# Optimization experiments

Measured on AMD Instinct MI355X. Metric: run time of the kernel, lower is better.

The kernel has to match this reference:

```python
import jax, jax.numpy as jnp
import numpy as np

N1, N2 = 8192, 4096
NUM_ITERS = 8  # bounded version of the data-dependent while-loop in Revision_PRED
EPS = 1e-6


def _make_boxes(key, n):
    k1, k2 = jax.random.split(key)
    lt = jax.random.uniform(k1, (n, 2), minval=0.0, maxval=800.0)
    wh = jax.random.uniform(k2, (n, 2), minval=1.0, maxval=200.0)
    return jnp.concatenate([lt, lt + wh], axis=1)  # valid xyxy boxes


def setup_inputs() -> dict:
    key = jax.random.key(0)
    ks = jax.random.split(key, 6)
    return {
        "bboxes1": _make_boxes(ks[0], N1),
        "scores1": jax.random.uniform(ks[1], (N1,)),
        "classes1": jax.random.randint(ks[2], (N1,), 0, 80),
        "bboxes2": _make_boxes(ks[3], N2),
        "scores2": jax.random.uniform(ks[4], (N2,)),
        "classes2": jax.random.randint(ks[5], (N2,), 0, 80),
    }


def bbox_overlaps_iou(b1, b2, eps=EPS):
    # b1: [N1,4], b2: [N2,4] xyxy -> [N1,N2] IoU (mode='iou', is_aligned=False)
    area1 = (b1[:, 2] - b1[:, 0]) * (b1[:, 3] - b1[:, 1])
    area2 = (b2[:, 2] - b2[:, 0]) * (b2[:, 3] - b2[:, 1])
    lt = jnp.maximum(b1[:, None, :2], b2[None, :, :2])
    rb = jnp.minimum(b1[:, None, 2:], b2[None, :, 2:])
    wh = jnp.clip(rb - lt, 0.0)
    overlap = wh[..., 0] * wh[..., 1]
    union = jnp.maximum(area1[:, None] + area2[None, :] - overlap, eps)
    return overlap / union


def reference(bboxes1, scores1, classes1, bboxes2, scores2, classes2):
    # Faithful JAX version of Revision_PRED: pairwise IoU + iterative
    # suppression (index_put_ of 0.5) + scatter of winning predictions.
    ious = bbox_overlaps_iou(bboxes1, bboxes2)
    cols = jnp.arange(ious.shape[1])

    def body(ious, _):
        refine_gt = (ious > 0.5).any(axis=0)            # [N2]
        refine_inds = jnp.argmax(ious, axis=0)          # [N2] best pred per box2
        need_refine = scores1[refine_inds] >= scores2
        lower = refine_gt & (~need_refine)              # == (~refine_gt|~need_refine)&refine_gt
        # index_put_ of 0.5 at (refine_inds[lower], lower cols); no-op elsewhere
        new_vals = jnp.where(lower, 0.5, ious[refine_inds, cols])
        ious = ious.at[refine_inds, cols].set(new_vals)
        return ious, None

    # Bounded, idempotent-once-converged replacement for the `while True` loop.
    ious, _ = jax.lax.scan(body, ious, None, length=NUM_ITERS)

    refine_gt = (ious > 0.5).any(axis=0)
    refine_inds = jnp.argmax(ious, axis=0)
    b2 = jnp.where(refine_gt[:, None], bboxes1[refine_inds], bboxes2)
    s2 = jnp.where(refine_gt, scores1[refine_inds], scores2)
    c2 = jnp.where(refine_gt, classes1[refine_inds], classes2)
    refined_boxes = (b2 + jnp.abs(b2)) * 0.5            # clamp negatives to 0
    missing_mask = (ious < 0.5).all(axis=1)             # preds kept as 'missing'
    return refined_boxes, s2, c2, missing_mask, ious
```

## Files before the change

### kernel.cpp

```cpp
#include <hip/hip_runtime.h>


typedef float vfloat4 __attribute__((ext_vector_type(4)));

constexpr int TOPK = 9;

__device__ __forceinline__ void key_insert(unsigned long long (&t)[TOPK],
                                           unsigned long long pk) {
    if (pk > t[TOPK - 1]) {
#pragma unroll
        for (int j = TOPK - 1; j >= 0; --j) {
            const bool gt_cur  = pk > t[j];
            const bool gt_prev = (j > 0) ? (pk > t[j - 1]) : false;
            if (gt_cur) t[j] = gt_prev ? t[j - 1] : pk;
        }
    }
}

__global__ __launch_bounds__(256) void iou_cand_kernel(
    const float* __restrict__ b1, const float* __restrict__ b2,
    float* __restrict__ ious,
    unsigned int* __restrict__ cnt, unsigned long long* __restrict__ cand,
    unsigned char* __restrict__ rowflag,
    int n1, int n2, int rps, int cap)
{
    const int tid = blockIdx.x * blockDim.x + threadIdx.x;
    const int c0 = tid * 4;
    if (c0 >= n2) return;
    const int r0 = blockIdx.y * rps;
    const int r1 = min(r0 + rps, n1);

    float4 bx[4]; float ar[4];
#pragma unroll
    for (int k = 0; k < 4; ++k) {
        bx[k] = reinterpret_cast<const float4*>(b2)[c0 + k];
        ar[k] = __fmul_rn(__fsub_rn(bx[k].z, bx[k].x),
                          __fsub_rn(bx[k].w, bx[k].y));
    }

    float* orow = ious + (size_t)r0 * n2 + c0;
    for (int r = r0; r < r1; ++r, orow += n2) {
        const float4 p = reinterpret_cast<const float4*>(b1)[r];
        const float a1 = __fmul_rn(__fsub_rn(p.z, p.x), __fsub_rn(p.w, p.y));
        float v[4], ovs[4], uns[4];
#pragma unroll
        for (int k = 0; k < 4; ++k) {
            const float wx = fmaxf(__fsub_rn(fminf(p.z, bx[k].z),
                                             fmaxf(p.x, bx[k].x)), 0.0f);
            const float wy = fmaxf(__fsub_rn(fminf(p.w, bx[k].w),
                                             fmaxf(p.y, bx[k].y)), 0.0f);
            const float ov = __fmul_rn(wx, wy);
            const float un = fmaxf(__fsub_rn(__fadd_rn(a1, ar[k]), ov), 1e-6f);
            ovs[k] = ov; uns[k] = un;
            float rc = __builtin_amdgcn_rcpf(un);
            rc = rc * fmaf(-un, rc, 2.0f);
            v[k] = ov * rc;
        }

        const float vmax = fmaxf(fmaxf(v[0], v[1]), fmaxf(v[2], v[3]));
        if (vmax > 0.499999f) {
#pragma unroll
            for (int k = 0; k < 4; ++k) {
                if (v[k] > 0.499999f) {
                    const float ve = __fdiv_rn(ovs[k], uns[k]);
                    v[k] = ve;
                    if (ve >= 0.5f) {
                        rowflag[r] = 1;
                        if (ve > 0.5f) {
                            const unsigned int idx = atomicAdd(&cnt[c0 + k], 1u);
                            if (idx < (unsigned int)cap)
                                cand[(size_t)idx * n2 + (c0 + k)] =
                                    ((unsigned long long)__float_as_uint(ve) << 32)
                                  | (unsigned long long)(~(unsigned int)r);
                        }
                    }
                }
            }
        }
        vfloat4 vo; vo.x = v[0]; vo.y = v[1]; vo.z = v[2]; vo.w = v[3];
        __builtin_nontemporal_store(vo, reinterpret_cast<vfloat4*>(orow));
    }
}

__global__ __launch_bounds__(64) void refine_missing_kernel(
    const float* __restrict__ b1, const float* __restrict__ s1,
    const int* __restrict__ c1,
    const float* __restrict__ b2, const float* __restrict__ s2,
    const int* __restrict__ c2,
    const unsigned int* __restrict__ cnt,
    const unsigned long long* __restrict__ cand,
    const unsigned char* __restrict__ rowflag,
    float* __restrict__ out_boxes, float* __restrict__ out_s,
    float* __restrict__ out_c, float* __restrict__ out_m,
    float* __restrict__ ious,
    int n1, int n2, int cap)
{
    const int tid = blockIdx.x * blockDim.x + threadIdx.x;

    if (tid < n1)
        out_m[tid] = rowflag[tid] ? 0.0f : 1.0f;

    const int c = tid;
    if (c >= n2) return;

    unsigned long long t[TOPK];
#pragma unroll
    for (int j = 0; j < TOPK; ++j) t[j] = 0ull;

    const int n = (int)cnt[c];
    if (n <= cap) {
        const unsigned long long* L = cand + c;
        for (int e = 0; e < n; ++e)
            key_insert(t, L[(size_t)e * n2]);
    } else {
        for (int r = 0; r < n1; ++r) {
            const float v = ious[(size_t)r * n2 + c];
            if (v > 0.5f)
                key_insert(t, ((unsigned long long)__float_as_uint(v) << 32)
                            | (unsigned long long)(~(unsigned int)r));
        }
    }

    int m = 0;
#pragma unroll
    for (int j = 0; j < TOPK; ++j) m += (t[j] != 0ull) ? 1 : 0;

    int   ti[TOPK];
    float s1v[TOPK];
    const float s2c = s2[c];
#pragma unroll
    for (int j = 0; j < TOPK; ++j) {
        ti[j]  = (int)~(unsigned int)(t[j] & 0xffffffffull);
        s1v[j] = (j < m) ? s1[ti[j]] : 0.0f;
    }

    int k = 0;
#pragma unroll
    for (int j = 0; j < 8; ++j)
        if (j < m && k == j && s1v[j] < s2c) k = j + 1;

#pragma unroll
    for (int j = 0; j < 8; ++j)
        if (j < k) ious[(size_t)ti[j] * n2 + c] = 0.5f;

    const bool refine = (k < m);
    int winner = 0; float wsc = 0.0f;
#pragma unroll
    for (int j = 0; j < TOPK; ++j)
        if (j == k) { winner = ti[j]; wsc = s1v[j]; }

    float4 ob; float os, oc;
    if (refine) {
        ob = reinterpret_cast<const float4*>(b1)[winner];
        os = wsc;
        oc = (float)c1[winner];
    } else {
        ob = reinterpret_cast<const float4*>(b2)[c];
        os = s2c;
        oc = (float)c2[c];
    }
    ob.x = fmaxf(ob.x, 0.0f); ob.y = fmaxf(ob.y, 0.0f);
    ob.z = fmaxf(ob.z, 0.0f); ob.w = fmaxf(ob.w, 0.0f);
    reinterpret_cast<float4*>(out_boxes)[c] = ob;
    out_s[c] = os;
    out_c[c] = oc;
}

extern "C" void kernel_launch(void* const* d_in, const int* in_sizes, int n_in,
                              void* d_out, int out_size, void* d_ws, size_t ws_size,
                              hipStream_t stream) {
    (void)n_in; (void)out_size;
    const float* b1 = (const float*)d_in[0];
    const float* s1 = (const float*)d_in[1];
    const int*   c1 = (const int*)d_in[2];
    const float* b2 = (const float*)d_in[3];
    const float* s2 = (const float*)d_in[4];
    const int*   c2 = (const int*)d_in[5];
    const int n1 = in_sizes[1];
    const int n2 = in_sizes[4];

    float* out       = (float*)d_out;
    float* out_boxes = out;
    float* out_s     = out + (size_t)n2 * 4;
    float* out_c     = out_s + n2;
    float* out_m     = out_c + n2;
    float* out_ious  = out_m + n1;

    const size_t cnt_b    = (size_t)n2 * sizeof(unsigned int);
    const size_t flag_b   = (size_t)n1;
    const size_t cand_off = (cnt_b + flag_b + 15) & ~(size_t)15;
    int cap = 1024;
    while (cap > 16 && cand_off + (size_t)cap * n2 * 8 > ws_size) cap >>= 1;
    unsigned int*       cnt     = (unsigned int*)d_ws;
    unsigned char*      rowflag = (unsigned char*)d_ws + cnt_b;
    unsigned long long* cand    = (unsigned long long*)((char*)d_ws + cand_off);

    (void)hipMemsetAsync(d_ws, 0, cnt_b + flag_b, stream);

    const int bx = (n2 / 4 + 255) / 256;
    int S = 2048 / bx; if (S < 1) S = 1; if (S > n1) S = n1;
    const int rps = (n1 + S - 1) / S;

    dim3 gridA(bx, S);
    iou_cand_kernel<<<gridA, 256, 0, stream>>>(b1, b2, out_ious, cnt, cand,
                                               rowflag, n1, n2, rps, cap);
    const int ntot = max(n1, n2);
    refine_missing_kernel<<<(ntot + 63) / 64, 64, 0, stream>>>(
        b1, s1, c1, b2, s2, c2, cnt, cand, rowflag,
        out_boxes, out_s, out_c, out_m, out_ious, n1, n2, cap);
}
```

Baseline: 54.29 us.

## Restructure IoU kernel to row-block tiling with two rows per pass

Each block now handles a small group of rows (four) and sweeps all columns, computing two rows per pass so that each b2 box load is reused across both rows. Before, each thread kept four b2 boxes in registers and looped over many rows. The grid goes from 2048 blocks to n1/4 blocks, and the nontemporal store becomes a normal store. This trades register-resident b2 reuse for reloading b2 per row pair, in exchange for contiguous full-row writes and more blocks in flight.

```diff
diff --git a/kernel.cpp b/kernel.cpp
--- a/kernel.cpp
+++ b/kernel.cpp
@@ -15,6 +15,49 @@
             if (gt_cur) t[j] = gt_prev ? t[j - 1] : pk;
         }
     }
+}
+
+__device__ __forceinline__ float4 iou4_row(
+    const float4 p, const float a1, const float4 (&bx)[4],
+    const float (&ar)[4], int c0, int r,
+    unsigned int* __restrict__ cnt, unsigned long long* __restrict__ cand,
+    unsigned char* __restrict__ rowflag, int n2, int cap)
+{
+    float v[4], ovs[4], uns[4];
+#pragma unroll
+    for (int k = 0; k < 4; ++k) {
+        const float wx = fmaxf(__fsub_rn(fminf(p.z, bx[k].z),
+                                         fmaxf(p.x, bx[k].x)), 0.0f);
+        const float wy = fmaxf(__fsub_rn(fminf(p.w, bx[k].w),
+                                         fmaxf(p.y, bx[k].y)), 0.0f);
+        const float ov = __fmul_rn(wx, wy);
+        const float un = fmaxf(__fsub_rn(__fadd_rn(a1, ar[k]), ov), 1e-6f);
+        ovs[k] = ov; uns[k] = un;
+        float rc = __builtin_amdgcn_rcpf(un);
+        rc = rc * fmaf(-un, rc, 2.0f);
+        v[k] = ov * rc;
+    }
+    const float vmax = fmaxf(fmaxf(v[0], v[1]), fmaxf(v[2], v[3]));
+    if (vmax > 0.499999f) {
+#pragma unroll
+        for (int k = 0; k < 4; ++k) {
+            if (v[k] > 0.499999f) {
+                const float ve = __fdiv_rn(ovs[k], uns[k]);
+                v[k] = ve;
+                if (ve >= 0.5f) {
+                    rowflag[r] = 1;
+                    if (ve > 0.5f) {
+                        const unsigned int idx = atomicAdd(&cnt[c0 + k], 1u);
+                        if (idx < (unsigned int)cap)
+                            cand[(size_t)idx * n2 + (c0 + k)] =
+                                ((unsigned long long)__float_as_uint(ve) << 32)
+                              | (unsigned long long)(~(unsigned int)r);
+                    }
+                }
+            }
+        }
+    }
+    return make_float4(v[0], v[1], v[2], v[3]);
 }
 
 __global__ __launch_bounds__(256) void iou_cand_kernel(
@@ -22,63 +65,46 @@
     float* __restrict__ ious,
     unsigned int* __restrict__ cnt, unsigned long long* __restrict__ cand,
     unsigned char* __restrict__ rowflag,
-    int n1, int n2, int rps, int cap)
+    int n1, int n2, int rpb, int cap)
 {
-    const int tid = blockIdx.x * blockDim.x + threadIdx.x;
-    const int c0 = tid * 4;
-    if (c0 >= n2) return;
-    const int r0 = blockIdx.y * rps;
-    const int r1 = min(r0 + rps, n1);
-
-    float4 bx[4]; float ar[4];
-#pragma unroll
-    for (int k = 0; k < 4; ++k) {
-        bx[k] = reinterpret_cast<const float4*>(b2)[c0 + k];
-        ar[k] = __fmul_rn(__fsub_rn(bx[k].z, bx[k].x),
-                          __fsub_rn(bx[k].w, bx[k].y));
-    }
-
-    float* orow = ious + (size_t)r0 * n2 + c0;
-    for (int r = r0; r < r1; ++r, orow += n2) {
-        const float4 p = reinterpret_cast<const float4*>(b1)[r];
-        const float a1 = __fmul_rn(__fsub_rn(p.z, p.x), __fsub_rn(p.w, p.y));
-        float v[4], ovs[4], uns[4];
-#pragma unroll
-        for (int k = 0; k < 4; ++k) {
-            const float wx = fmaxf(__fsub_rn(fminf(p.z, bx[k].z),
-                                             fmaxf(p.x, bx[k].x)), 0.0f);
-            const float wy = fmaxf(__fsub_rn(fminf(p.w, bx[k].w),
-                                             fmaxf(p.y, bx[k].y)), 0.0f);
-            const float ov = __fmul_rn(wx, wy);
-            const float un = fmaxf(__fsub_rn(__fadd_rn(a1, ar[k]), ov), 1e-6f);
-            ovs[k] = ov; uns[k] = un;
-            float rc = __builtin_amdgcn_rcpf(un);
-            rc = rc * fmaf(-un, rc, 2.0f);
-            v[k] = ov * rc;
-        }
-
-        const float vmax = fmaxf(fmaxf(v[0], v[1]), fmaxf(v[2], v[3]));
-        if (vmax > 0.499999f) {
+    const int tx = threadIdx.x;
+    const int r0 = blockIdx.x * rpb;
+    const int cpp = blockDim.x * 4;
+
+    for (int rp = 0; rp < rpb; rp += 2) {
+        const int r = r0 + rp;
+        if (r >= n1) return;
+        const bool two = (rp + 1 < rpb) && (r + 1 < n1);
+
+        const float4 pA = reinterpret_cast<const float4*>(b1)[r];
+        const float a1A = __fmul_rn(__fsub_rn(pA.z, pA.x),
+                                    __fsub_rn(pA.w, pA.y));
+        float4 pB = pA; float a1B = a1A;
+        if (two) {
+            pB  = reinterpret_cast<const float4*>(b1)[r + 1];
+            a1B = __fmul_rn(__fsub_rn(pB.z, pB.x), __fsub_rn(pB.w, pB.y));
+        }
+
+        float* rowA = ious + (size_t)r * n2;
+        float* rowB = ious + (size_t)(r + 1) * n2;
+
+        for (int c0 = tx * 4; c0 < n2; c0 += cpp) {
+            float4 bx[4]; float ar[4];
 #pragma unroll
             for (int k = 0; k < 4; ++k) {
-                if (v[k] > 0.499999f) {
-                    const float ve = __fdiv_rn(ovs[k], uns[k]);
-                    v[k] = ve;
-                    if (ve >= 0.5f) {
-                        rowflag[r] = 1;
-                        if (ve > 0.5f) {
-                            const unsigned int idx = atomicAdd(&cnt[c0 + k], 1u);
-                            if (idx < (unsigned int)cap)
-                                cand[(size_t)idx * n2 + (c0 + k)] =
-                                    ((unsigned long long)__float_as_uint(ve) << 32)
-                                  | (unsigned long long)(~(unsigned int)r);
-                        }
-                    }
-                }
+                bx[k] = reinterpret_cast<const float4*>(b2)[c0 + k];
+                ar[k] = __fmul_rn(__fsub_rn(bx[k].z, bx[k].x),
+                                  __fsub_rn(bx[k].w, bx[k].y));
             }
-        }
-        vfloat4 vo; vo.x = v[0]; vo.y = v[1]; vo.z = v[2]; vo.w = v[3];
-        __builtin_nontemporal_store(vo, reinterpret_cast<vfloat4*>(orow));
+            const float4 vA = iou4_row(pA, a1A, bx, ar, c0, r,
+                                       cnt, cand, rowflag, n2, cap);
+            *reinterpret_cast<float4*>(rowA + c0) = vA;
+            if (two) {
+                const float4 vB = iou4_row(pB, a1B, bx, ar, c0, r + 1,
+                                           cnt, cand, rowflag, n2, cap);
+                *reinterpret_cast<float4*>(rowB + c0) = vB;
+            }
+        }
     }
 }
 
@@ -197,13 +223,10 @@
 
     (void)hipMemsetAsync(d_ws, 0, cnt_b + flag_b, stream);
 
-    const int bx = (n2 / 4 + 255) / 256;
-    int S = 2048 / bx; if (S < 1) S = 1; if (S > n1) S = n1;
-    const int rps = (n1 + S - 1) / S;
-
-    dim3 gridA(bx, S);
-    iou_cand_kernel<<<gridA, 256, 0, stream>>>(b1, b2, out_ious, cnt, cand,
-                                               rowflag, n1, n2, rps, cap);
+    const int rpb = 4;
+    const int nblk = (n1 + rpb - 1) / rpb;
+    iou_cand_kernel<<<nblk, 256, 0, stream>>>(b1, b2, out_ious, cnt, cand,
+                                              rowflag, n1, n2, rpb, cap);
     const int ntot = max(n1, n2);
     refine_missing_kernel<<<(ntot + 63) / 64, 64, 0, stream>>>(
         b1, s1, c1, b2, s2, c2, cnt, cand, rowflag,
```

Result: no change. 55.21 us (+1.7%).
